# Kernel optimization log

Measured on AMD Instinct MI355X. Metric: run time of the kernel, lower is better.

## Reference

```python
import jax, jax.numpy as jnp
import numpy as np

THRESHOLD = 0.5


def _crop_resize(img, hstart, ch, wstart, cw, out_h, out_w):
    # Bilinear resample (TF half-pixel-centers) of the crop
    # img[hstart:hstart+ch, wstart:wstart+cw] up to (out_h, out_w).
    chf = ch.astype(jnp.float32)
    cwf = cw.astype(jnp.float32)
    ys = jnp.clip((jnp.arange(out_h, dtype=jnp.float32) + 0.5) * (chf / out_h) - 0.5,
                  0.0, chf - 1.0) + hstart
    xs = jnp.clip((jnp.arange(out_w, dtype=jnp.float32) + 0.5) * (cwf / out_w) - 0.5,
                  0.0, cwf - 1.0) + wstart
    y0 = jnp.floor(ys).astype(jnp.int32)
    y1 = jnp.minimum(y0 + 1, hstart + ch - 1)
    x0 = jnp.floor(xs).astype(jnp.int32)
    x1 = jnp.minimum(x0 + 1, wstart + cw - 1)
    wy = (ys - y0)[:, None, None]
    wx = (xs - x0)[None, :, None]
    r0 = img[y0]  # (out_h, W, C) gathered rows
    r1 = img[y1]
    top = (1.0 - wx) * r0[:, x0] + wx * r0[:, x1]
    bot = (1.0 - wx) * r1[:, x0] + wx * r1[:, x1]
    return (1.0 - wy) * top + wy * bot


def _per_sample(mask, img):
    H, W = img.shape[0], img.shape[1]
    m = (mask >= THRESHOLD).astype(img.dtype)  # (H, W, 1)
    masked = m * img                           # (H, W, C)
    rows = jnp.sum(m[..., 0], axis=1)          # row sums (H,)
    cols = jnp.sum(m[..., 0], axis=0)          # col sums (W,)
    # bbox: first nonzero index - 1 (clamped to 0), last nonzero index + 1
    xl = jnp.maximum(jnp.argmax(rows > 0).astype(jnp.int32) - 1, 0)
    xr = (H - jnp.argmax((rows > 0)[::-1])).astype(jnp.int32)
    yl = jnp.maximum(jnp.argmax(cols > 0).astype(jnp.int32) - 1, 0)
    yr = (W - jnp.argmax((cols > 0)[::-1])).astype(jnp.int32)
    h = xr - xl
    w = yr - yl
    # smart_resize with square target: center-crop bbox to square side min(h, w)
    c = jnp.minimum(h, w)
    hstart = xl + (h - c) // 2
    wstart = yl + (w - c) // 2
    return _crop_resize(masked, hstart, c, wstart, c, H, W)


def setup_inputs() -> dict:
    key = jax.random.key(0)
    k1, k2 = jax.random.split(key)
    masks = jax.random.uniform(k1, (16, 1024, 1024, 1), dtype=jnp.float32)
    images = jax.random.uniform(k2, (16, 1024, 1024, 3), dtype=jnp.float32)
    return {"masks": masks, "images": images}


def reference(masks, images):
    return jax.vmap(_per_sample)(masks, images)
```

## Files before the change

kernel.cpp:

```cpp
#include <hip/hip_runtime.h>

#define HH 1024
#define WW 1024
#define NS 16
#define RB 4

typedef float f32x4 __attribute__((ext_vector_type(4)));

__global__ __launch_bounds__(256)
void fused_kernel(const float* __restrict__ mask,
                  const float* __restrict__ img,
                  int* __restrict__ rowMinC,
                  int* __restrict__ rowMaxC,
                  float* __restrict__ out) {
    const int s  = blockIdx.y;
    const int r0 = blockIdx.x * RB;
    const int t  = threadIdx.x;

    const f32x4* m4 = (const f32x4*)(mask + (size_t)s * HH * WW);
    __shared__ unsigned int pw[RB][32];
    __shared__ int smin[RB][4], smax[RB][4];

    for (int rr = 0; rr < RB; ++rr) {
        const int row = r0 + rr;
        f32x4 v = __builtin_nontemporal_load(&m4[(size_t)row * 256 + t]);
        unsigned int w = (v.x >= 0.5f ? 1u : 0u)
                       | (v.y >= 0.5f ? 2u : 0u)
                       | (v.z >= 0.5f ? 4u : 0u)
                       | (v.w >= 0.5f ? 8u : 0u);
        w |= __shfl_down(w, 1) << 4;
        w |= __shfl_down(w, 2) << 8;
        w |= __shfl_down(w, 4) << 16;

        int cmin = WW, cmax = -1;
        if ((t & 7) == 0) {
            int g = t >> 3;
            pw[rr][g] = w;
            if (w) {
                cmin = (g << 5) + __builtin_ctz(w);
                cmax = (g << 5) + 31 - __builtin_clz(w);
            }
        }
        for (int off = 32; off > 0; off >>= 1) {
            cmin = min(cmin, __shfl_down(cmin, off));
            cmax = max(cmax, __shfl_down(cmax, off));
        }
        if ((t & 63) == 0) { smin[rr][t >> 6] = cmin; smax[rr][t >> 6] = cmax; }
    }
    __syncthreads();
    if (t < RB) {
        int cmin = min(min(smin[t][0], smin[t][1]), min(smin[t][2], smin[t][3]));
        int cmax = max(max(smax[t][0], smax[t][1]), max(smax[t][2], smax[t][3]));
        rowMinC[s * HH + r0 + t] = cmin;
        rowMaxC[s * HH + r0 + t] = cmax;
    }

    const f32x4* ip = (const f32x4*)(img + ((size_t)s * HH + r0) * WW * 3);
    f32x4*       op = (f32x4*)(out + ((size_t)s * HH + r0) * WW * 3);
    for (int rr = 0; rr < RB; ++rr) {
        const unsigned int* pwr = pw[rr];
#pragma unroll
        for (int j = 0; j < 3; ++j) {
            int fi = t + (j << 8);
            int F  = fi << 2;
            int p0 = F / 3;
            int r  = F - p0 * 3;
            unsigned int b0 = (pwr[p0 >> 5] >> (p0 & 31)) & 1u;
            int p1 = p0 + 1;
            unsigned int b1 = (pwr[p1 >> 5] >> (p1 & 31)) & 1u;
            size_t off = (size_t)rr * 768 + fi;
            f32x4 v = __builtin_nontemporal_load(&ip[off]);
            f32x4 o;
            o.x = b0 ? v.x : 0.0f;
            o.y = ((r < 2) ? b0 : b1) ? v.y : 0.0f;
            o.z = ((r == 0) ? b0 : b1) ? v.z : 0.0f;
            o.w = b1 ? v.w : 0.0f;
            __builtin_nontemporal_store(o, &op[off]);
        }
    }
}

__global__ __launch_bounds__(256)
void reduce_kernel(const int* __restrict__ rowMinC,
                   const int* __restrict__ rowMaxC,
                   int* __restrict__ bc4) {
    const int s = blockIdx.x;
    const int t = threadIdx.x;
    int minR = HH, maxR = -1, minC = WW, maxC = -1;
#pragma unroll
    for (int m = 0; m < HH / 256; ++m) {
        int r = t + (m << 8);
        int mc = rowMaxC[s * HH + r];
        if (mc >= 0) {
            minR = min(minR, r);
            maxR = max(maxR, r);
            minC = min(minC, rowMinC[s * HH + r]);
            maxC = max(maxC, mc);
        }
    }
    for (int off = 32; off > 0; off >>= 1) {
        minR = min(minR, __shfl_down(minR, off));
        maxR = max(maxR, __shfl_down(maxR, off));
        minC = min(minC, __shfl_down(minC, off));
        maxC = max(maxC, __shfl_down(maxC, off));
    }
    __shared__ int sm[4][4];
    int wave = t >> 6, lane = t & 63;
    if (lane == 0) { sm[wave][0] = minR; sm[wave][1] = maxR; sm[wave][2] = minC; sm[wave][3] = maxC; }
    __syncthreads();
    if (t == 0) {
        for (int wv = 1; wv < 4; ++wv) {
            minR = min(minR, sm[wv][0]);
            maxR = max(maxR, sm[wv][1]);
            minC = min(minC, sm[wv][2]);
            maxC = max(maxC, sm[wv][3]);
        }
        int xl, xr, yl, yr;
        if (maxR < 0) { xl = 0; xr = HH; } else { xl = max(minR - 1, 0); xr = maxR + 1; }
        if (maxC < 0) { yl = 0; yr = WW; } else { yl = max(minC - 1, 0); yr = maxC + 1; }
        int h = xr - xl, w = yr - yl;
        int c = min(h, w);
        bc4[s * 4 + 0] = c;
        bc4[s * 4 + 1] = xl + (h - c) / 2;
        bc4[s * 4 + 2] = yl + (w - c) / 2;
        bc4[s * 4 + 3] = 0;
    }
}

__global__ __launch_bounds__(256)
void fixup_kernel(const float* __restrict__ mask,
                  const float* __restrict__ img,
                  const int* __restrict__ bc4,
                  float* __restrict__ out) {
    const int s  = blockIdx.y;
    const int c      = bc4[s * 4 + 0];
    const int hstart = bc4[s * 4 + 1];
    const int wstart = bc4[s * 4 + 2];
    if (c == HH && hstart == 0 && wstart == 0) return;

    const int r0 = blockIdx.x * RB;
    const int t  = threadIdx.x;
    const float* msk = mask + (size_t)s * HH * WW;
    const float* im  = img  + (size_t)s * HH * WW * 3;
    float*       ob  = out  + (size_t)s * HH * WW * 3;

    float cf = (float)c;
    float sy = cf / (float)HH;
    float sx = cf / (float)WW;

    for (int rr = 0; rr < RB; ++rr) {
        const int row = r0 + rr;
        float ysf = fminf(fmaxf((row + 0.5f) * sy - 0.5f, 0.0f), cf - 1.0f);
        int   y0i = (int)floorf(ysf);
        float wy  = ysf - (float)y0i;
        int   ry0 = hstart + y0i;
        int   ry1 = min(ry0 + 1, hstart + c - 1);
        float* orow = ob + (size_t)row * WW * 3;

        for (int k = 0; k < 4; ++k) {
            int ox = (t << 2) + k;
            float xsf = fminf(fmaxf((ox + 0.5f) * sx - 0.5f, 0.0f), cf - 1.0f);
            int   x0i = (int)floorf(xsf);
            float wx  = xsf - (float)x0i;
            int   rx0 = wstart + x0i;
            int   rx1 = min(rx0 + 1, wstart + c - 1);

            float p00[3], p01[3], p10[3], p11[3];
            auto fetch = [&](int y, int x, float* p) {
                int idx = y * WW + x;
                float mv = msk[idx];
                if (mv >= 0.5f) {
                    const float* q = im + (size_t)idx * 3;
                    p[0] = q[0]; p[1] = q[1]; p[2] = q[2];
                } else {
                    p[0] = 0.0f; p[1] = 0.0f; p[2] = 0.0f;
                }
            };
            fetch(ry0, rx0, p00);
            fetch(ry0, rx1, p01);
            fetch(ry1, rx0, p10);
            fetch(ry1, rx1, p11);

            float* o = orow + (size_t)ox * 3;
#pragma unroll
            for (int ch = 0; ch < 3; ++ch) {
                float top = (1.0f - wx) * p00[ch] + wx * p01[ch];
                float bot = (1.0f - wx) * p10[ch] + wx * p11[ch];
                o[ch] = (1.0f - wy) * top + wy * bot;
            }
        }
    }
}

extern "C" void kernel_launch(void* const* d_in, const int* in_sizes, int n_in,
                              void* d_out, int out_size, void* d_ws, size_t ws_size,
                              hipStream_t stream) {
    const float* masks  = (const float*)d_in[0];
    const float* images = (const float*)d_in[1];
    float* out = (float*)d_out;

    int* rowMinC = (int*)d_ws;
    int* rowMaxC = rowMinC + NS * HH;
    int* bc4     = rowMaxC + NS * HH;

    fused_kernel <<<dim3(HH / RB, NS), 256, 0, stream>>>(masks, images, rowMinC, rowMaxC, out);
    reduce_kernel<<<NS,                256, 0, stream>>>(rowMinC, rowMaxC, bc4);
    fixup_kernel <<<dim3(HH / RB, NS), 256, 0, stream>>>(masks, images, bc4, out);
}
```

Measured before the change: 88.88 us.

## Batch mask and image loads up front and merge reduce with fixup kernel

The fused kernel now issues all mask and image vector loads for its four rows before any compute, which raises memory-level parallelism per thread at the cost of more registers. The separate reduce and fixup kernels are merged into one tail kernel with one block per sample. That block computes the bounding box into shared memory and, if a crop is needed, loops over all 1024 rows itself. This removes a launch and the bc4 round trip through global memory. The risk is that a non-identity crop would then be resampled by only 16 blocks, which is very slow. With uniform random masks the bbox almost always covers the whole image, so that path exits early.

```diff
diff --git a/kernel.cpp b/kernel.cpp
--- a/kernel.cpp
+++ b/kernel.cpp
@@ -18,16 +18,30 @@
     const int t  = threadIdx.x;
 
     const f32x4* m4 = (const f32x4*)(mask + (size_t)s * HH * WW);
+    const f32x4* ip = (const f32x4*)(img + ((size_t)s * HH + r0) * WW * 3);
+    f32x4*       op = (f32x4*)(out + ((size_t)s * HH + r0) * WW * 3);
+
+    f32x4 mv[RB];
+#pragma unroll
+    for (int rr = 0; rr < RB; ++rr)
+        mv[rr] = __builtin_nontemporal_load(&m4[(size_t)(r0 + rr) * 256 + t]);
+
+    f32x4 iv[RB][3];
+#pragma unroll
+    for (int rr = 0; rr < RB; ++rr)
+#pragma unroll
+        for (int j = 0; j < 3; ++j)
+            iv[rr][j] = __builtin_nontemporal_load(&ip[(size_t)rr * 768 + t + (j << 8)]);
+
     __shared__ unsigned int pw[RB][32];
     __shared__ int smin[RB][4], smax[RB][4];
 
+#pragma unroll
     for (int rr = 0; rr < RB; ++rr) {
-        const int row = r0 + rr;
-        f32x4 v = __builtin_nontemporal_load(&m4[(size_t)row * 256 + t]);
-        unsigned int w = (v.x >= 0.5f ? 1u : 0u)
-                       | (v.y >= 0.5f ? 2u : 0u)
-                       | (v.z >= 0.5f ? 4u : 0u)
-                       | (v.w >= 0.5f ? 8u : 0u);
+        unsigned int w = (mv[rr].x >= 0.5f ? 1u : 0u)
+                       | (mv[rr].y >= 0.5f ? 2u : 0u)
+                       | (mv[rr].z >= 0.5f ? 4u : 0u)
+                       | (mv[rr].w >= 0.5f ? 8u : 0u);
         w |= __shfl_down(w, 1) << 4;
         w |= __shfl_down(w, 2) << 8;
         w |= __shfl_down(w, 4) << 16;
@@ -55,8 +69,7 @@
         rowMaxC[s * HH + r0 + t] = cmax;
     }
 
-    const f32x4* ip = (const f32x4*)(img + ((size_t)s * HH + r0) * WW * 3);
-    f32x4*       op = (f32x4*)(out + ((size_t)s * HH + r0) * WW * 3);
+#pragma unroll
     for (int rr = 0; rr < RB; ++rr) {
         const unsigned int* pwr = pw[rr];
 #pragma unroll
@@ -68,24 +81,26 @@
             unsigned int b0 = (pwr[p0 >> 5] >> (p0 & 31)) & 1u;
             int p1 = p0 + 1;
             unsigned int b1 = (pwr[p1 >> 5] >> (p1 & 31)) & 1u;
-            size_t off = (size_t)rr * 768 + fi;
-            f32x4 v = __builtin_nontemporal_load(&ip[off]);
+            f32x4 v = iv[rr][j];
             f32x4 o;
             o.x = b0 ? v.x : 0.0f;
             o.y = ((r < 2) ? b0 : b1) ? v.y : 0.0f;
             o.z = ((r == 0) ? b0 : b1) ? v.z : 0.0f;
             o.w = b1 ? v.w : 0.0f;
-            __builtin_nontemporal_store(o, &op[off]);
+            __builtin_nontemporal_store(o, &op[(size_t)rr * 768 + fi]);
         }
     }
 }
 
 __global__ __launch_bounds__(256)
-void reduce_kernel(const int* __restrict__ rowMinC,
-                   const int* __restrict__ rowMaxC,
-                   int* __restrict__ bc4) {
+void tail_kernel(const float* __restrict__ mask,
+                 const float* __restrict__ img,
+                 const int* __restrict__ rowMinC,
+                 const int* __restrict__ rowMaxC,
+                 float* __restrict__ out) {
     const int s = blockIdx.x;
     const int t = threadIdx.x;
+
     int minR = HH, maxR = -1, minC = WW, maxC = -1;
 #pragma unroll
     for (int m = 0; m < HH / 256; ++m) {
@@ -105,6 +120,7 @@
         maxC = max(maxC, __shfl_down(maxC, off));
     }
     __shared__ int sm[4][4];
+    __shared__ int bc[3];
     int wave = t >> 6, lane = t & 63;
     if (lane == 0) { sm[wave][0] = minR; sm[wave][1] = maxR; sm[wave][2] = minC; sm[wave][3] = maxC; }
     __syncthreads();
@@ -120,26 +136,14 @@
         if (maxC < 0) { yl = 0; yr = WW; } else { yl = max(minC - 1, 0); yr = maxC + 1; }
         int h = xr - xl, w = yr - yl;
         int c = min(h, w);
-        bc4[s * 4 + 0] = c;
-        bc4[s * 4 + 1] = xl + (h - c) / 2;
-        bc4[s * 4 + 2] = yl + (w - c) / 2;
-        bc4[s * 4 + 3] = 0;
-    }
-}
-
-__global__ __launch_bounds__(256)
-void fixup_kernel(const float* __restrict__ mask,
-                  const float* __restrict__ img,
-                  const int* __restrict__ bc4,
-                  float* __restrict__ out) {
-    const int s  = blockIdx.y;
-    const int c      = bc4[s * 4 + 0];
-    const int hstart = bc4[s * 4 + 1];
-    const int wstart = bc4[s * 4 + 2];
+        bc[0] = c;
+        bc[1] = xl + (h - c) / 2;
+        bc[2] = yl + (w - c) / 2;
+    }
+    __syncthreads();
+    const int c = bc[0], hstart = bc[1], wstart = bc[2];
     if (c == HH && hstart == 0 && wstart == 0) return;
 
-    const int r0 = blockIdx.x * RB;
-    const int t  = threadIdx.x;
     const float* msk = mask + (size_t)s * HH * WW;
     const float* im  = img  + (size_t)s * HH * WW * 3;
     float*       ob  = out  + (size_t)s * HH * WW * 3;
@@ -148,8 +152,7 @@
     float sy = cf / (float)HH;
     float sx = cf / (float)WW;
 
-    for (int rr = 0; rr < RB; ++rr) {
-        const int row = r0 + rr;
+    for (int row = 0; row < HH; ++row) {
         float ysf = fminf(fmaxf((row + 0.5f) * sy - 0.5f, 0.0f), cf - 1.0f);
         int   y0i = (int)floorf(ysf);
         float wy  = ysf - (float)y0i;
@@ -201,9 +204,7 @@
 
     int* rowMinC = (int*)d_ws;
     int* rowMaxC = rowMinC + NS * HH;
-    int* bc4     = rowMaxC + NS * HH;
-
-    fused_kernel <<<dim3(HH / RB, NS), 256, 0, stream>>>(masks, images, rowMinC, rowMaxC, out);
-    reduce_kernel<<<NS,                256, 0, stream>>>(rowMinC, rowMaxC, bc4);
-    fixup_kernel <<<dim3(HH / RB, NS), 256, 0, stream>>>(masks, images, bc4, out);
+
+    fused_kernel<<<dim3(HH / RB, NS), 256, 0, stream>>>(masks, images, rowMinC, rowMaxC, out);
+    tail_kernel <<<NS,                256, 0, stream>>>(masks, images, rowMinC, rowMaxC, out);
 }
```

Result: faster. 84.94 us (-4.4%).
